# Performance work log

Measured on AMD Instinct MI355X. Metric: run time of the kernel, lower is better.

The kernel has to match this reference:

```python
import jax, jax.numpy as jnp
import numpy as np

IN_FEATURES = 512
OUT_FEATURES = 512
BATCH = 1024


def setup_inputs() -> dict:
    key = jax.random.key(0)
    k_x, k_bw, k_ww, k_sc, k_tr, k_b = jax.random.split(key, 6)
    std = 1.0 / np.sqrt(IN_FEATURES)
    x = jax.random.normal(k_x, (BATCH, IN_FEATURES), dtype=jnp.float32)
    base_weight = jax.random.uniform(k_bw, (OUT_FEATURES, IN_FEATURES), jnp.float32, -std, std)
    wavelet_weights = jax.random.uniform(k_ww, (OUT_FEATURES, IN_FEATURES), jnp.float32, -std, std)
    # scale initialized to ones in the module; perturb slightly (kept positive) for a non-degenerate test
    scale = jnp.exp(0.1 * jax.random.normal(k_sc, (OUT_FEATURES, IN_FEATURES), dtype=jnp.float32))
    translation = 0.1 * jax.random.normal(k_tr, (OUT_FEATURES, IN_FEATURES), dtype=jnp.float32)
    bias = jax.random.uniform(k_b, (OUT_FEATURES,), jnp.float32, -std, std)
    return {"x": x, "base_weight": base_weight, "wavelet_weights": wavelet_weights,
            "scale": scale, "translation": translation, "bias": bias}


def reference(x, base_weight, wavelet_weights, scale, translation, bias):
    # base branch: SiLU then linear
    base_out = jnp.einsum("bi,oi->bo", jax.nn.silu(x), base_weight)
    # wavelet branch: broadcast x to (batch, out, in)
    xs = (x[:, None, :] - translation[None, :, :]) / scale[None, :, :]  # (B, O, I)
    wavelet = (xs * xs - 1.0) * jnp.exp(-0.5 * xs * xs)  # mexican hat
    wavelet_out = jnp.einsum("boi,oi->bo", wavelet, wavelet_weights)
    return base_out + wavelet_out + bias
```

## Files before the change

### kernel.cpp

```cpp
#include <hip/hip_runtime.h>


constexpr int IN_F  = 512;
constexpr int OUT_F = 512;
constexpr int BATCH = 1024;
constexpr int BT = 128, OT = 64;
constexpr int KS = 8;
constexpr int KR = IN_F / KS;
constexpr int IT = 16;
constexpr int PITCH = IT + 4;
constexpr int NCH = KR / IT;
constexpr int BO  = BATCH * OUT_F;

#define LOG2E 1.44269504088897f
#define C2f   (-0.72134752044448f)
#define NC2f  ( 0.72134752044448f)
#define RQf   (-0.84083003f)

typedef float v2f __attribute__((ext_vector_type(2)));

__device__ __forceinline__ float fexp2(float v) { return __builtin_amdgcn_exp2f(v); }
__device__ __forceinline__ float frcp(float v)  { return __builtin_amdgcn_rcpf(v); }
__device__ __forceinline__ v2f pkfma(v2f a, v2f b, v2f c) {
  return __builtin_elementwise_fma(a, b, c);
}
__device__ __forceinline__ float fsilu(float v) {
  return v * frcp(1.f + fexp2(v * -LOG2E));
}

__global__ __launch_bounds__(256, 2)
void wkan_main(const float* __restrict__ x, const float* __restrict__ basew,
               const float* __restrict__ wavew, const float* __restrict__ scale,
               const float* __restrict__ transl, const float* __restrict__ bias,
               float* __restrict__ partial, float* __restrict__ out, int use_ws)
{
  __shared__ float lx [BT * PITCH];
  __shared__ float lsx[BT * PITCH];
  __shared__ float la [OT * PITCH];
  __shared__ float lm [OT * PITCH];
  __shared__ float ln [OT * PITCH];
  __shared__ float lq [OT * PITCH];
  __shared__ float lb [OT * PITCH];

  const int tid = threadIdx.x;
  const int b0 = blockIdx.x * BT;
  const int o0 = blockIdx.y * OT;
  const int ks = blockIdx.z;
  const int k0 = ks * KR;

  const int srow = tid >> 2;
  const int sc4  = (tid & 3) * 4;
  const int lofs = srow * PITCH + sc4;

  const int to = tid & 15;
  const int tb = tid >> 4;

  v2f zz; zz.x = 0.f; zz.y = 0.f;
  v2f acc[8][4];
#pragma unroll
  for (int r = 0; r < 8; ++r)
#pragma unroll
    for (int c = 0; c < 4; ++c) acc[r][c] = zz;

  float4 xv0, xv1, sv, tv, wv, bv;

  {
    const int g = k0 + sc4;
    xv0 = *(const float4*)(x      + (size_t)(b0 + srow)      * IN_F + g);
    xv1 = *(const float4*)(x      + (size_t)(b0 + srow + 64) * IN_F + g);
    sv  = *(const float4*)(scale  + (size_t)(o0 + srow) * IN_F + g);
    tv  = *(const float4*)(transl + (size_t)(o0 + srow) * IN_F + g);
    wv  = *(const float4*)(wavew  + (size_t)(o0 + srow) * IN_F + g);
    bv  = *(const float4*)(basew  + (size_t)(o0 + srow) * IN_F + g);
  }

  for (int kc = 0; kc < NCH; ++kc) {
    if (kc) __syncthreads();
    {
      float4 sx0, sx1;
      sx0.x = fsilu(xv0.x); sx0.y = fsilu(xv0.y); sx0.z = fsilu(xv0.z); sx0.w = fsilu(xv0.w);
      sx1.x = fsilu(xv1.x); sx1.y = fsilu(xv1.y); sx1.z = fsilu(xv1.z); sx1.w = fsilu(xv1.w);
      *(float4*)(lx  + lofs) = xv0;
      *(float4*)(lsx + lofs) = sx0;
      *(float4*)(lx  + lofs + 64 * PITCH) = xv1;
      *(float4*)(lsx + lofs + 64 * PITCH) = sx1;

      float4 av, mv, nv;
      {
        float a2, a2t;
        a2 = C2f * frcp(sv.x * sv.x); a2t = a2 * tv.x;
        av.x = a2; mv.x = -2.f * a2t; nv.x = fmaf(a2t, tv.x, NC2f);
        a2 = C2f * frcp(sv.y * sv.y); a2t = a2 * tv.y;
        av.y = a2; mv.y = -2.f * a2t; nv.y = fmaf(a2t, tv.y, NC2f);
        a2 = C2f * frcp(sv.z * sv.z); a2t = a2 * tv.z;
        av.z = a2; mv.z = -2.f * a2t; nv.z = fmaf(a2t, tv.z, NC2f);
        a2 = C2f * frcp(sv.w * sv.w); a2t = a2 * tv.w;
        av.w = a2; mv.w = -2.f * a2t; nv.w = fmaf(a2t, tv.w, NC2f);
      }
      *(float4*)(la + lofs) = av;
      *(float4*)(lm + lofs) = mv;
      *(float4*)(ln + lofs) = nv;

      float4 qv;
      qv.x = wv.x * RQf; qv.y = wv.y * RQf; qv.z = wv.z * RQf; qv.w = wv.w * RQf;
      *(float4*)(lq + lofs) = qv;
      *(float4*)(lb + lofs) = bv;
    }
    __syncthreads();

    if (kc + 1 < NCH) {
      const int g = k0 + (kc + 1) * IT + sc4;
      xv0 = *(const float4*)(x      + (size_t)(b0 + srow)      * IN_F + g);
      xv1 = *(const float4*)(x      + (size_t)(b0 + srow + 64) * IN_F + g);
      sv  = *(const float4*)(scale  + (size_t)(o0 + srow) * IN_F + g);
      tv  = *(const float4*)(transl + (size_t)(o0 + srow) * IN_F + g);
      wv  = *(const float4*)(wavew  + (size_t)(o0 + srow) * IN_F + g);
      bv  = *(const float4*)(basew  + (size_t)(o0 + srow) * IN_F + g);
    }

    for (int ii = 0; ii < IT; ii += 4) {
      float4 xr[8], sr[8], x2[8];
#pragma unroll
      for (int r = 0; r < 8; ++r) {
        const int row = (tb + 16 * r) * PITCH + ii;
        xr[r] = *(const float4*)(lx + row);
        sr[r] = *(const float4*)(lsx + row);
        x2[r].x = xr[r].x * xr[r].x;
        x2[r].y = xr[r].y * xr[r].y;
        x2[r].z = xr[r].z * xr[r].z;
        x2[r].w = xr[r].w * xr[r].w;
      }
#pragma unroll
      for (int c = 0; c < 4; ++c) {
        const int orow = (to + 16 * c) * PITCH + ii;
        float4 A = *(const float4*)(la + orow);
        float4 M = *(const float4*)(lm + orow);
        float4 N = *(const float4*)(ln + orow);
        float4 Q = *(const float4*)(lq + orow);
        float4 B = *(const float4*)(lb + orow);
        v2f Al = {A.x, A.y}, Ah = {A.z, A.w};
        v2f Ml = {M.x, M.y}, Mh = {M.z, M.w};
        v2f Nl = {N.x, N.y}, Nh = {N.z, N.w};
        v2f Ql = {Q.x, Q.y}, Qh = {Q.z, Q.w};
        v2f Bl = {B.x, B.y}, Bh = {B.z, B.w};
#pragma unroll
        for (int r = 0; r < 8; ++r) {
          v2f xl  = {xr[r].x, xr[r].y}, xh  = {xr[r].z, xr[r].w};
          v2f x2l = {x2[r].x, x2[r].y}, x2h = {x2[r].z, x2[r].w};
          v2f sl  = {sr[r].x, sr[r].y}, sh  = {sr[r].z, sr[r].w};
          v2f p, e, gg;
          p = pkfma(Al, x2l, pkfma(Ml, xl, Nl));
          e.x = fexp2(p.x); e.y = fexp2(p.y);
          gg = p * Ql;
          acc[r][c] = pkfma(gg, e, acc[r][c]);
          acc[r][c] = pkfma(sl, Bl, acc[r][c]);
          p = pkfma(Ah, x2h, pkfma(Mh, xh, Nh));
          e.x = fexp2(p.x); e.y = fexp2(p.y);
          gg = p * Qh;
          acc[r][c] = pkfma(gg, e, acc[r][c]);
          acc[r][c] = pkfma(sh, Bh, acc[r][c]);
        }
      }
    }
  }

#pragma unroll
  for (int r = 0; r < 8; ++r) {
    const int br = b0 + tb + 16 * r;
#pragma unroll
    for (int c = 0; c < 4; ++c) {
      const int oc = o0 + to + 16 * c;
      float res = acc[r][c].x + acc[r][c].y;
      if (use_ws) {
        partial[(size_t)ks * BO + (size_t)br * OUT_F + oc] = res;
      } else {
        if (ks == 0) res += bias[oc];
        atomicAdd(out + (size_t)br * OUT_F + oc, res);
      }
    }
  }
}

__global__ __launch_bounds__(256)
void wkan_reduce(const float* __restrict__ partial, const float* __restrict__ bias,
                 float* __restrict__ out)
{
  const int i4 = (blockIdx.x * 256 + threadIdx.x) * 4;
  float4 r = *(const float4*)(bias + (i4 & (OUT_F - 1)));
#pragma unroll
  for (int k = 0; k < KS; ++k) {
    float4 a = *(const float4*)(partial + (size_t)k * BO + i4);
    r.x += a.x; r.y += a.y; r.z += a.z; r.w += a.w;
  }
  *(float4*)(out + i4) = r;
}

extern "C" void kernel_launch(void* const* d_in, const int* in_sizes, int n_in,
                              void* d_out, int out_size, void* d_ws, size_t ws_size,
                              hipStream_t stream) {
  const float* x  = (const float*)d_in[0];
  const float* bw = (const float*)d_in[1];
  const float* ww = (const float*)d_in[2];
  const float* sc = (const float*)d_in[3];
  const float* tr = (const float*)d_in[4];
  const float* bi = (const float*)d_in[5];
  float* out = (float*)d_out;

  const int use_ws = ws_size >= (size_t)KS * BO * sizeof(float) ? 1 : 0;
  if (!use_ws) {
    hipMemsetAsync(d_out, 0, (size_t)out_size * sizeof(float), stream);
  }
  dim3 grid(BATCH / BT, OUT_F / OT, KS);
  wkan_main<<<grid, dim3(256), 0, stream>>>(x, bw, ww, sc, tr, bi,
                                            (float*)d_ws, out, use_ws);
  if (use_ws) {
    wkan_reduce<<<dim3(BO / 1024), dim3(256), 0, stream>>>((const float*)d_ws, bi, out);
  }
}
```

Measured before the change: 114.8 us.

## Move SiLU base-branch matmul onto fp16 MFMA instructions

The SiLU·base_weight product is taken out of the scalar packed-FMA inner loop and computed with 16x16x16 fp16 MFMA instructions. SiLU(x) and base_weight are staged in shared memory as fp16. The MFMA results are written to a shared buffer at the end and added to the wavelet accumulators before output. This removes two packed FMAs per element pair and two LDS streams from the VALU-bound loop, at the cost of fp16 input precision, extra shared memory that may affect occupancy, and an extra sync.

```diff
diff --git a/kernel.cpp b/kernel.cpp
--- a/kernel.cpp
+++ b/kernel.cpp
@@ -9,6 +9,8 @@
 constexpr int KR = IN_F / KS;
 constexpr int IT = 16;
 constexpr int PITCH = IT + 4;
+constexpr int HP = IT + 4;
+constexpr int LP = OT + 1;
 constexpr int NCH = KR / IT;
 constexpr int BO  = BATCH * OUT_F;
 
@@ -17,7 +19,9 @@
 #define NC2f  ( 0.72134752044448f)
 #define RQf   (-0.84083003f)
 
-typedef float v2f __attribute__((ext_vector_type(2)));
+typedef float v2f   __attribute__((ext_vector_type(2)));
+typedef float f32x4 __attribute__((ext_vector_type(4)));
+typedef _Float16 half4 __attribute__((ext_vector_type(4)));
 
 __device__ __forceinline__ float fexp2(float v) { return __builtin_amdgcn_exp2f(v); }
 __device__ __forceinline__ float frcp(float v)  { return __builtin_amdgcn_rcpf(v); }
@@ -35,12 +39,13 @@
                float* __restrict__ partial, float* __restrict__ out, int use_ws)
 {
   __shared__ float lx [BT * PITCH];
-  __shared__ float lsx[BT * PITCH];
   __shared__ float la [OT * PITCH];
   __shared__ float lm [OT * PITCH];
   __shared__ float ln [OT * PITCH];
   __shared__ float lq [OT * PITCH];
-  __shared__ float lb [OT * PITCH];
+  __shared__ _Float16 hx [BT * HP];
+  __shared__ _Float16 hb [OT * HP];
+  __shared__ float lout[BT * LP];
 
   const int tid = threadIdx.x;
   const int b0 = blockIdx.x * BT;
@@ -51,10 +56,16 @@
   const int srow = tid >> 2;
   const int sc4  = (tid & 3) * 4;
   const int lofs = srow * PITCH + sc4;
+  const int hofs = srow * HP + sc4;
 
   const int to = tid & 15;
   const int tb = tid >> 4;
 
+  const int lane = tid & 63;
+  const int wid  = tid >> 6;
+  const int frow = lane & 15;
+  const int kgrp = (lane >> 4) * 4;
+
   v2f zz; zz.x = 0.f; zz.y = 0.f;
   v2f acc[8][4];
 #pragma unroll
@@ -62,8 +73,13 @@
 #pragma unroll
     for (int c = 0; c < 4; ++c) acc[r][c] = zz;
 
+  f32x4 accb[2][4];
+#pragma unroll
+  for (int mt = 0; mt < 2; ++mt)
+#pragma unroll
+    for (int nt = 0; nt < 4; ++nt) accb[mt][nt] = (f32x4)0.f;
+
   float4 xv0, xv1, sv, tv, wv, bv;
-
   {
     const int g = k0 + sc4;
     xv0 = *(const float4*)(x      + (size_t)(b0 + srow)      * IN_F + g);
@@ -80,10 +96,15 @@
       float4 sx0, sx1;
       sx0.x = fsilu(xv0.x); sx0.y = fsilu(xv0.y); sx0.z = fsilu(xv0.z); sx0.w = fsilu(xv0.w);
       sx1.x = fsilu(xv1.x); sx1.y = fsilu(xv1.y); sx1.z = fsilu(xv1.z); sx1.w = fsilu(xv1.w);
-      *(float4*)(lx  + lofs) = xv0;
-      *(float4*)(lsx + lofs) = sx0;
-      *(float4*)(lx  + lofs + 64 * PITCH) = xv1;
-      *(float4*)(lsx + lofs + 64 * PITCH) = sx1;
+      *(float4*)(lx + lofs) = xv0;
+      *(float4*)(lx + lofs + 64 * PITCH) = xv1;
+      half4 h0, h1;
+      h0[0] = (_Float16)sx0.x; h0[1] = (_Float16)sx0.y;
+      h0[2] = (_Float16)sx0.z; h0[3] = (_Float16)sx0.w;
+      h1[0] = (_Float16)sx1.x; h1[1] = (_Float16)sx1.y;
+      h1[2] = (_Float16)sx1.z; h1[3] = (_Float16)sx1.w;
+      *(half4*)(hx + hofs) = h0;
+      *(half4*)(hx + hofs + 64 * HP) = h1;
 
       float4 av, mv, nv;
       {
@@ -104,7 +125,11 @@
       float4 qv;
       qv.x = wv.x * RQf; qv.y = wv.y * RQf; qv.z = wv.z * RQf; qv.w = wv.w * RQf;
       *(float4*)(lq + lofs) = qv;
-      *(float4*)(lb + lofs) = bv;
+
+      half4 hbv;
+      hbv[0] = (_Float16)bv.x; hbv[1] = (_Float16)bv.y;
+      hbv[2] = (_Float16)bv.z; hbv[3] = (_Float16)bv.w;
+      *(half4*)(hb + hofs) = hbv;
     }
     __syncthreads();
 
@@ -118,13 +143,23 @@
       bv  = *(const float4*)(basew  + (size_t)(o0 + srow) * IN_F + g);
     }
 
+    {
+      half4 af0 = *(const half4*)(hx + (wid * 32 +      frow) * HP + kgrp);
+      half4 af1 = *(const half4*)(hx + (wid * 32 + 16 + frow) * HP + kgrp);
+#pragma unroll
+      for (int nt = 0; nt < 4; ++nt) {
+        half4 bf = *(const half4*)(hb + (nt * 16 + frow) * HP + kgrp);
+        accb[0][nt] = __builtin_amdgcn_mfma_f32_16x16x16f16(af0, bf, accb[0][nt], 0, 0, 0);
+        accb[1][nt] = __builtin_amdgcn_mfma_f32_16x16x16f16(af1, bf, accb[1][nt], 0, 0, 0);
+      }
+    }
+
     for (int ii = 0; ii < IT; ii += 4) {
-      float4 xr[8], sr[8], x2[8];
+      float4 xr[8], x2[8];
 #pragma unroll
       for (int r = 0; r < 8; ++r) {
         const int row = (tb + 16 * r) * PITCH + ii;
         xr[r] = *(const float4*)(lx + row);
-        sr[r] = *(const float4*)(lsx + row);
         x2[r].x = xr[r].x * xr[r].x;
         x2[r].y = xr[r].y * xr[r].y;
         x2[r].z = xr[r].z * xr[r].z;
@@ -137,32 +172,37 @@
         float4 M = *(const float4*)(lm + orow);
         float4 N = *(const float4*)(ln + orow);
         float4 Q = *(const float4*)(lq + orow);
-        float4 B = *(const float4*)(lb + orow);
         v2f Al = {A.x, A.y}, Ah = {A.z, A.w};
         v2f Ml = {M.x, M.y}, Mh = {M.z, M.w};
         v2f Nl = {N.x, N.y}, Nh = {N.z, N.w};
         v2f Ql = {Q.x, Q.y}, Qh = {Q.z, Q.w};
-        v2f Bl = {B.x, B.y}, Bh = {B.z, B.w};
 #pragma unroll
         for (int r = 0; r < 8; ++r) {
           v2f xl  = {xr[r].x, xr[r].y}, xh  = {xr[r].z, xr[r].w};
           v2f x2l = {x2[r].x, x2[r].y}, x2h = {x2[r].z, x2[r].w};
-          v2f sl  = {sr[r].x, sr[r].y}, sh  = {sr[r].z, sr[r].w};
           v2f p, e, gg;
           p = pkfma(Al, x2l, pkfma(Ml, xl, Nl));
           e.x = fexp2(p.x); e.y = fexp2(p.y);
           gg = p * Ql;
           acc[r][c] = pkfma(gg, e, acc[r][c]);
-          acc[r][c] = pkfma(sl, Bl, acc[r][c]);
           p = pkfma(Ah, x2h, pkfma(Mh, xh, Nh));
           e.x = fexp2(p.x); e.y = fexp2(p.y);
           gg = p * Qh;
           acc[r][c] = pkfma(gg, e, acc[r][c]);
-          acc[r][c] = pkfma(sh, Bh, acc[r][c]);
         }
       }
     }
   }
+
+#pragma unroll
+  for (int mt = 0; mt < 2; ++mt)
+#pragma unroll
+    for (int nt = 0; nt < 4; ++nt)
+#pragma unroll
+      for (int i = 0; i < 4; ++i)
+        lout[(wid * 32 + mt * 16 + (lane >> 4) * 4 + i) * LP + nt * 16 + frow]
+            = accb[mt][nt][i];
+  __syncthreads();
 
 #pragma unroll
   for (int r = 0; r < 8; ++r) {
@@ -170,7 +210,8 @@
 #pragma unroll
     for (int c = 0; c < 4; ++c) {
       const int oc = o0 + to + 16 * c;
-      float res = acc[r][c].x + acc[r][c].y;
+      float res = acc[r][c].x + acc[r][c].y
+                + lout[(tb + 16 * r) * LP + to + 16 * c];
       if (use_ws) {
         partial[(size_t)ks * BO + (size_t)br * OUT_F + oc] = res;
       } else {
```

After: 111.1 us. 1.03x faster.
